# Kernel optimization log

Hardware: AMD Instinct MI355X
Metric: run time of the kernel (lower is better)

## Reference

```python
import jax, jax.numpy as jnp
import numpy as np

B, T, D_IN, EMB, H = 2, 2048, 1024, 1024, 16
HD = EMB // H  # head_dim = 64


def setup_inputs() -> dict:
    key = jax.random.key(0)
    ks = jax.random.split(key, 3)
    scale_qkv = 1.0 / np.sqrt(D_IN)
    scale_o = 1.0 / np.sqrt(EMB)
    return {
        "x": jax.random.normal(ks[0], (B, T, D_IN), dtype=jnp.float32),
        "W_qkv": jax.random.normal(ks[1], (D_IN, 3 * EMB), dtype=jnp.float32) * scale_qkv,
        "b_qkv": jnp.zeros((3 * EMB,), dtype=jnp.float32),
        "W_o": jax.random.normal(ks[2], (EMB, EMB), dtype=jnp.float32) * scale_o,
        "b_o": jnp.zeros((EMB,), dtype=jnp.float32),
    }


def reference(x, W_qkv, b_qkv, W_o, b_o):
    b, t, _ = x.shape
    qkv = x @ W_qkv + b_qkv                      # [B,T,3*EMB]
    # Match torch: reshape to (B,T,H,3*HD) -> permute -> chunk into q,k,v
    qkv = qkv.reshape(b, t, H, 3 * HD).transpose(0, 2, 1, 3)  # [B,H,T,3*HD]
    q, k, v = jnp.split(qkv, 3, axis=-1)         # each [B,H,T,HD]
    scale = 1.0 / jnp.sqrt(jnp.asarray(HD, dtype=q.dtype))
    scores = jnp.einsum("bhqd,bhkd->bhqk", q, k) * scale  # [B,H,T,T]
    attn = jax.nn.softmax(scores, axis=-1)
    values = jnp.einsum("bhqk,bhkd->bhqd", attn, v)       # [B,H,T,HD]
    values = values.transpose(0, 2, 1, 3).reshape(b, t, EMB)
    return values @ W_o + b_o
```

## Files before the change

### kernel.cpp

```cpp
#include <hip/hip_runtime.h>
#include <math.h>

typedef __bf16 bf16x8 __attribute__((ext_vector_type(8)));
typedef float f32x4 __attribute__((ext_vector_type(4)));
typedef short s16x4 __attribute__((ext_vector_type(4)));

#define GPTR(p) ((const __attribute__((address_space(1))) void*)(p))
#define LPTR(p) ((__attribute__((address_space(3))) void*)(p))

#define QSCALE 0.18033688011112042f

__device__ __forceinline__ unsigned short f2bf(float f) {
  unsigned int u = __float_as_uint(f);
  u += 0x7FFFu + ((u >> 16) & 1u);
  return (unsigned short)(u >> 16);
}

__device__ __forceinline__ unsigned int pack_bf2(float lo, float hi) {
  return __builtin_amdgcn_perm(__float_as_uint(hi) + 0x8000u,
                               __float_as_uint(lo) + 0x8000u, 0x07060302u);
}

__device__ __forceinline__ float fast_exp2(float x) {
#if __has_builtin(__builtin_amdgcn_exp2f)
  return __builtin_amdgcn_exp2f(x);
#else
  return exp2f(x);
#endif
}

__device__ __forceinline__ f32x4 zero4() {
  f32x4 z; z[0] = 0.f; z[1] = 0.f; z[2] = 0.f; z[3] = 0.f; return z;
}

__global__ void conv_x_bf16(const float* __restrict__ in, unsigned short* __restrict__ out) {
  int i = (blockIdx.x * 256 + threadIdx.x) * 4;
  float4 v = *(const float4*)(in + i);
  ushort4 o;
  o.x = f2bf(v.x); o.y = f2bf(v.y); o.z = f2bf(v.z); o.w = f2bf(v.w);
  *(ushort4*)(out + i) = o;
}

__global__ void transpose_conv(const float* __restrict__ in, unsigned short* __restrict__ out,
                               int K, int N) {
  __shared__ float tile[64][65];
  int k0 = blockIdx.y * 64, n0 = blockIdx.x * 64;
  int t = threadIdx.x;
#pragma unroll
  for (int p = 0; p < 16; ++p) {
    int l = p * 256 + t; int r = l >> 6, c = l & 63;
    tile[r][c] = in[(size_t)(k0 + r) * N + n0 + c];
  }
  __syncthreads();
#pragma unroll
  for (int p = 0; p < 16; ++p) {
    int l = p * 256 + t; int r = l >> 6, c = l & 63;
    out[(size_t)(n0 + r) * K + k0 + c] = f2bf(tile[c][r]);
  }
}

__global__ __launch_bounds__(256) void gemm_qkv(
    const unsigned short* __restrict__ A, const unsigned short* __restrict__ Bt,
    const float* __restrict__ bias,
    unsigned short* __restrict__ Qd, unsigned short* __restrict__ Kd,
    unsigned short* __restrict__ Vtd) {
  __shared__ unsigned short As[128 * 32];
  __shared__ unsigned short Bs[128 * 32];
  const int tid = threadIdx.x, wave = tid >> 6, lane = tid & 63;
  const int quad = lane >> 4, l16 = lane & 15;
  const int wm = (wave >> 1) * 64, wn = (wave & 1) * 64;
  const int m0 = blockIdx.y * 128, n0 = blockIdx.x * 128;
  f32x4 acc[4][4];
#pragma unroll
  for (int i = 0; i < 4; ++i)
#pragma unroll
    for (int j = 0; j < 4; ++j) acc[i][j] = zero4();

  const int c = wave * 64 + lane;
  const int rA = c >> 2, o16 = (c & 3) * 8;

  for (int k0 = 0; k0 < 1024; k0 += 32) {
    __syncthreads();
    __builtin_amdgcn_global_load_lds(GPTR(A + (size_t)(m0 + rA) * 1024 + k0 + o16),
                                     LPTR(As + wave * 512), 16, 0, 0);
    __builtin_amdgcn_global_load_lds(GPTR(A + (size_t)(m0 + 64 + rA) * 1024 + k0 + o16),
                                     LPTR(As + 2048 + wave * 512), 16, 0, 0);
    __builtin_amdgcn_global_load_lds(GPTR(Bt + (size_t)(n0 + rA) * 1024 + k0 + o16),
                                     LPTR(Bs + wave * 512), 16, 0, 0);
    __builtin_amdgcn_global_load_lds(GPTR(Bt + (size_t)(n0 + 64 + rA) * 1024 + k0 + o16),
                                     LPTR(Bs + 2048 + wave * 512), 16, 0, 0);
    __syncthreads();
    bf16x8 af[4], bfr[4];
#pragma unroll
    for (int mt = 0; mt < 4; ++mt)
      af[mt] = *(const bf16x8*)(As + (wm + mt * 16 + l16) * 32 + quad * 8);
#pragma unroll
    for (int nt = 0; nt < 4; ++nt)
      bfr[nt] = *(const bf16x8*)(Bs + (wn + nt * 16 + l16) * 32 + quad * 8);
#pragma unroll
    for (int mt = 0; mt < 4; ++mt)
#pragma unroll
      for (int nt = 0; nt < 4; ++nt)
        acc[mt][nt] = __builtin_amdgcn_mfma_f32_16x16x32_bf16(af[mt], bfr[nt], acc[mt][nt], 0, 0, 0);
  }

#pragma unroll
  for (int mt = 0; mt < 4; ++mt) {
#pragma unroll
    for (int nt = 0; nt < 4; ++nt) {
      int m = m0 + wm + mt * 16 + quad * 4;
      int n = n0 + wn + nt * 16 + l16;
      float bv = bias[n];
      int h = n / 192, rem = n - h * 192;
      int which = rem >> 6, d = rem & 63;
      int b = m >> 11, t0 = m & 2047;
      size_t head = (size_t)(b * 16 + h);
      f32x4 a = acc[mt][nt];
      if (which == 0) {
        size_t base = (head * 2048 + t0) * 64 + d;
#pragma unroll
        for (int i = 0; i < 4; ++i)
          Qd[base + (size_t)i * 64] = f2bf((a[i] + bv) * QSCALE);
      } else if (which == 1) {
        size_t base = head * 131072 + (size_t)(t0 >> 6) * 4096;
#pragma unroll
        for (int i = 0; i < 4; ++i) {
          int tt = t0 + i;
          Kd[base + (tt & 63) * 64 + (((d >> 3) ^ (tt & 7)) << 3) + (d & 7)] = f2bf(a[i] + bv);
        }
      } else {
        size_t base = head * 131072 + (size_t)(t0 >> 6) * 4096;
        ushort4 o;
        o.x = f2bf(a[0] + bv); o.y = f2bf(a[1] + bv);
        o.z = f2bf(a[2] + bv); o.w = f2bf(a[3] + bv);
        *(ushort4*)(Vtd + base + d * 64 + (((((t0 & 63) >> 3)) ^ (d & 7)) << 3) + (t0 & 7)) = o;
      }
    }
  }
}

__global__ __launch_bounds__(256) void flash_attn(
    const unsigned short* __restrict__ Qg,
    const unsigned short* __restrict__ Kg,
    const unsigned short* __restrict__ Vg,
    unsigned short* __restrict__ att) {
  __shared__ __align__(16) char smem[33792];
  unsigned short* Tb = (unsigned short*)smem;
  float* redO = (float*)smem;
  float* redL = (float*)(smem + 32768);
  const int tid = threadIdx.x, wave = tid >> 6, lane = tid & 63;
  const int quad = lane >> 4, l16 = lane & 15;
  const int h7 = l16 & 7;
  const int qhalf = wave >> 1, kh2 = wave & 1;
  const int bh = blockIdx.y;
  const int q0 = blockIdx.x * 128 + qhalf * 64;

  bf16x8 bq[4][2];
#pragma unroll
  for (int qg = 0; qg < 4; ++qg)
#pragma unroll
    for (int kh = 0; kh < 2; ++kh)
      bq[qg][kh] = *(const bf16x8*)(Qg + ((size_t)bh * 2048 + q0 + qg * 16 + l16) * 64 + kh * 32 + quad * 8);

  f32x4 o[4][4];
#pragma unroll
  for (int mt = 0; mt < 4; ++mt)
#pragma unroll
    for (int qg = 0; qg < 4; ++qg) o[mt][qg] = zero4();
  float lacc[4] = {0.f, 0.f, 0.f, 0.f};

  const unsigned short* Kt = Kg + (size_t)bh * 131072 + lane * 8;
  const unsigned short* Vt = Vg + (size_t)bh * 131072 + lane * 8;

  {
    unsigned short* Kb = Tb;
    __builtin_amdgcn_global_load_lds(GPTR(Kt + wave * 512),          LPTR(Kb + wave * 512), 16, 0, 0);
    __builtin_amdgcn_global_load_lds(GPTR(Kt + (4 + wave) * 512),    LPTR(Kb + (4 + wave) * 512), 16, 0, 0);
    __builtin_amdgcn_global_load_lds(GPTR(Vt + wave * 512),          LPTR(Kb + 4096 + wave * 512), 16, 0, 0);
    __builtin_amdgcn_global_load_lds(GPTR(Vt + (4 + wave) * 512),    LPTR(Kb + 4096 + (4 + wave) * 512), 16, 0, 0);
  }

  for (int tile = 0; tile < 32; ++tile) {
    __syncthreads();
    if (tile + 1 < 32) {
      unsigned short* Kb = Tb + ((tile + 1) & 1) * 8192;
      const unsigned short* Kg1 = Kt + (tile + 1) * 4096;
      const unsigned short* Vg1 = Vt + (tile + 1) * 4096;
      __builtin_amdgcn_global_load_lds(GPTR(Kg1 + wave * 512),       LPTR(Kb + wave * 512), 16, 0, 0);
      __builtin_amdgcn_global_load_lds(GPTR(Kg1 + (4 + wave) * 512), LPTR(Kb + (4 + wave) * 512), 16, 0, 0);
      __builtin_amdgcn_global_load_lds(GPTR(Vg1 + wave * 512),       LPTR(Kb + 4096 + wave * 512), 16, 0, 0);
      __builtin_amdgcn_global_load_lds(GPTR(Vg1 + (4 + wave) * 512), LPTR(Kb + 4096 + (4 + wave) * 512), 16, 0, 0);
    }
    const unsigned short* Ks = Tb + (tile & 1) * 8192;
    const unsigned short* Vs = Ks + 4096;

    f32x4 s[4][2];
#pragma unroll
    for (int qg = 0; qg < 4; ++qg)
#pragma unroll
      for (int kt = 0; kt < 2; ++kt) s[qg][kt] = zero4();
#pragma unroll
    for (int kt = 0; kt < 2; ++kt) {
      int krow = kh2 * 32 + kt * 16 + l16;
#pragma unroll
      for (int kh = 0; kh < 2; ++kh) {
        bf16x8 a = *(const bf16x8*)(Ks + krow * 64 + (((kh * 4 + quad) ^ h7) << 3));
#pragma unroll
        for (int qg = 0; qg < 4; ++qg)
          s[qg][kt] = __builtin_amdgcn_mfma_f32_16x16x32_bf16(a, bq[qg][kh], s[qg][kt], 0, 0, 0);
      }
    }

#pragma unroll
    for (int kt = 0; kt < 2; ++kt) {
      s16x4 pB[4];
#pragma unroll
      for (int qg = 0; qg < 4; ++qg) {
        float p0 = fast_exp2(s[qg][kt][0]);
        float p1 = fast_exp2(s[qg][kt][1]);
        float p2 = fast_exp2(s[qg][kt][2]);
        float p3 = fast_exp2(s[qg][kt][3]);
        lacc[qg] += (p0 + p1) + (p2 + p3);
        union { unsigned int u[2]; s16x4 v; } pk;
        pk.u[0] = pack_bf2(p0, p1);
        pk.u[1] = pack_bf2(p2, p3);
        pB[qg] = pk.v;
      }
      int cV = kh2 * 4 + kt * 2 + (quad >> 1);
#pragma unroll
      for (int mt = 0; mt < 4; ++mt) {
        s16x4 aV = *(const s16x4*)(Vs + (mt * 16 + l16) * 64 + ((cV ^ h7) << 3) + (quad & 1) * 4);
#pragma unroll
        for (int qg = 0; qg < 4; ++qg)
          o[mt][qg] = __builtin_amdgcn_mfma_f32_16x16x16bf16_1k(aV, pB[qg], o[mt][qg], 0, 0, 0);
      }
    }
  }

  float lfull[4];
#pragma unroll
  for (int qg = 0; qg < 4; ++qg) {
    float lw = lacc[qg];
    lw += __shfl_xor(lw, 16);
    lw += __shfl_xor(lw, 32);
    lfull[qg] = lw;
  }
  __syncthreads();
  if (kh2 == 1) {
    float* ob = redO + qhalf * 4096;
#pragma unroll
    for (int mt = 0; mt < 4; ++mt)
#pragma unroll
      for (int qg = 0; qg < 4; ++qg)
        *(f32x4*)(ob + ((qg * 4 + mt) * 4 + quad) * 64 + l16 * 4) = o[mt][qg];
    if (quad == 0) {
#pragma unroll
      for (int qg = 0; qg < 4; ++qg)
        redL[qhalf * 64 + qg * 16 + l16] = lfull[qg];
    }
  }
  __syncthreads();
  if (kh2 == 0) {
    int b = bh >> 4, h = bh & 15;
    float* ob = redO + qhalf * 4096;
#pragma unroll
    for (int qg = 0; qg < 4; ++qg) {
      float linv = 1.f / (lfull[qg] + redL[qhalf * 64 + qg * 16 + l16]);
      unsigned short* orow = att + ((size_t)b * 2048 + q0 + qg * 16 + l16) * 1024 + h * 64;
#pragma unroll
      for (int mt = 0; mt < 4; ++mt) {
        f32x4 part = *(const f32x4*)(ob + ((qg * 4 + mt) * 4 + quad) * 64 + l16 * 4);
        ushort4 ov;
        ov.x = f2bf((o[mt][qg][0] + part[0]) * linv);
        ov.y = f2bf((o[mt][qg][1] + part[1]) * linv);
        ov.z = f2bf((o[mt][qg][2] + part[2]) * linv);
        ov.w = f2bf((o[mt][qg][3] + part[3]) * linv);
        *(ushort4*)(orow + mt * 16 + quad * 4) = ov;
      }
    }
  }
}

__global__ __launch_bounds__(256) void gemm_out(
    const unsigned short* __restrict__ A, const unsigned short* __restrict__ Bt,
    const float* __restrict__ bias, float* __restrict__ out) {
  __shared__ unsigned short As[128 * 32];
  __shared__ unsigned short Bs[128 * 32];
  const int tid = threadIdx.x, wave = tid >> 6, lane = tid & 63;
  const int quad = lane >> 4, l16 = lane & 15;
  const int wm = (wave >> 1) * 64, wn = (wave & 1) * 64;
  const int m0 = blockIdx.y * 128, n0 = blockIdx.x * 128;
  f32x4 acc[4][4];
#pragma unroll
  for (int i = 0; i < 4; ++i)
#pragma unroll
    for (int j = 0; j < 4; ++j) acc[i][j] = zero4();

  const int c = wave * 64 + lane;
  const int rA = c >> 2, o16 = (c & 3) * 8;

  for (int k0 = 0; k0 < 1024; k0 += 32) {
    __syncthreads();
    __builtin_amdgcn_global_load_lds(GPTR(A + (size_t)(m0 + rA) * 1024 + k0 + o16),
                                     LPTR(As + wave * 512), 16, 0, 0);
    __builtin_amdgcn_global_load_lds(GPTR(A + (size_t)(m0 + 64 + rA) * 1024 + k0 + o16),
                                     LPTR(As + 2048 + wave * 512), 16, 0, 0);
    __builtin_amdgcn_global_load_lds(GPTR(Bt + (size_t)(n0 + rA) * 1024 + k0 + o16),
                                     LPTR(Bs + wave * 512), 16, 0, 0);
    __builtin_amdgcn_global_load_lds(GPTR(Bt + (size_t)(n0 + 64 + rA) * 1024 + k0 + o16),
                                     LPTR(Bs + 2048 + wave * 512), 16, 0, 0);
    __syncthreads();
    bf16x8 af[4], bfr[4];
#pragma unroll
    for (int mt = 0; mt < 4; ++mt)
      af[mt] = *(const bf16x8*)(As + (wm + mt * 16 + l16) * 32 + quad * 8);
#pragma unroll
    for (int nt = 0; nt < 4; ++nt)
      bfr[nt] = *(const bf16x8*)(Bs + (wn + nt * 16 + l16) * 32 + quad * 8);
#pragma unroll
    for (int mt = 0; mt < 4; ++mt)
#pragma unroll
      for (int nt = 0; nt < 4; ++nt)
        acc[mt][nt] = __builtin_amdgcn_mfma_f32_16x16x32_bf16(af[mt], bfr[nt], acc[mt][nt], 0, 0, 0);
  }

#pragma unroll
  for (int mt = 0; mt < 4; ++mt) {
#pragma unroll
    for (int nt = 0; nt < 4; ++nt) {
      int m = m0 + wm + mt * 16 + quad * 4;
      int n = n0 + wn + nt * 16 + l16;
      float bv = bias[n];
      float* orow = out + (size_t)m * 1024 + n;
      orow[0]        = acc[mt][nt][0] + bv;
      orow[1024]     = acc[mt][nt][1] + bv;
      orow[2 * 1024] = acc[mt][nt][2] + bv;
      orow[3 * 1024] = acc[mt][nt][3] + bv;
    }
  }
}

extern "C" void kernel_launch(void* const* d_in, const int* in_sizes, int n_in,
                              void* d_out, int out_size, void* d_ws, size_t ws_size,
                              hipStream_t stream) {
  const float* x    = (const float*)d_in[0];
  const float* Wqkv = (const float*)d_in[1];
  const float* bqkv = (const float*)d_in[2];
  const float* Wo   = (const float*)d_in[3];
  const float* bo   = (const float*)d_in[4];
  float* out = (float*)d_out;

  unsigned short* xb    = (unsigned short*)d_ws;
  unsigned short* wqkvt = xb    + (size_t)4096 * 1024;
  unsigned short* wot   = wqkvt + (size_t)3072 * 1024;
  unsigned short* Qd    = wot   + (size_t)1024 * 1024;
  unsigned short* Kd    = Qd    + (size_t)32 * 2048 * 64;
  unsigned short* Vtd   = Kd    + (size_t)32 * 2048 * 64;
  unsigned short* attb  = Vtd   + (size_t)32 * 2048 * 64;

  conv_x_bf16<<<4096, 256, 0, stream>>>(x, xb);
  transpose_conv<<<dim3(48, 16), 256, 0, stream>>>(Wqkv, wqkvt, 1024, 3072);
  transpose_conv<<<dim3(16, 16), 256, 0, stream>>>(Wo, wot, 1024, 1024);
  gemm_qkv<<<dim3(24, 32), 256, 0, stream>>>(xb, wqkvt, bqkv, Qd, Kd, Vtd);
  flash_attn<<<dim3(16, 32), 256, 0, stream>>>(Qd, Kd, Vtd, attb);
  gemm_out<<<dim3(8, 32), 256, 0, stream>>>(attb, wot, bo, out);
}
```

Measured before the change: 219.9 us.

## Split flash attention over key range with atomic fp32 partials and combine kernel

New measurement: 502.7 us. 2.29x slower.

```diff
diff --git a/kernel.cpp b/kernel.cpp
--- a/kernel.cpp
+++ b/kernel.cpp
@@ -139,11 +139,12 @@
   }
 }
 
-__global__ __launch_bounds__(256) void flash_attn(
+__global__ __launch_bounds__(256, 4) void flash_attn(
     const unsigned short* __restrict__ Qg,
     const unsigned short* __restrict__ Kg,
     const unsigned short* __restrict__ Vg,
-    unsigned short* __restrict__ att) {
+    float* __restrict__ pO,
+    float* __restrict__ pL) {
   __shared__ __align__(16) char smem[33792];
   unsigned short* Tb = (unsigned short*)smem;
   float* redO = (float*)smem;
@@ -154,6 +155,7 @@
   const int qhalf = wave >> 1, kh2 = wave & 1;
   const int bh = blockIdx.y;
   const int q0 = blockIdx.x * 128 + qhalf * 64;
+  const int tstart = blockIdx.z * 16, tend = tstart + 16;
 
   bf16x8 bq[4][2];
 #pragma unroll
@@ -173,16 +175,18 @@
   const unsigned short* Vt = Vg + (size_t)bh * 131072 + lane * 8;
 
   {
-    unsigned short* Kb = Tb;
-    __builtin_amdgcn_global_load_lds(GPTR(Kt + wave * 512),          LPTR(Kb + wave * 512), 16, 0, 0);
-    __builtin_amdgcn_global_load_lds(GPTR(Kt + (4 + wave) * 512),    LPTR(Kb + (4 + wave) * 512), 16, 0, 0);
-    __builtin_amdgcn_global_load_lds(GPTR(Vt + wave * 512),          LPTR(Kb + 4096 + wave * 512), 16, 0, 0);
-    __builtin_amdgcn_global_load_lds(GPTR(Vt + (4 + wave) * 512),    LPTR(Kb + 4096 + (4 + wave) * 512), 16, 0, 0);
-  }
-
-  for (int tile = 0; tile < 32; ++tile) {
-    __syncthreads();
-    if (tile + 1 < 32) {
+    unsigned short* Kb = Tb + (tstart & 1) * 8192;
+    const unsigned short* Kg0 = Kt + tstart * 4096;
+    const unsigned short* Vg0 = Vt + tstart * 4096;
+    __builtin_amdgcn_global_load_lds(GPTR(Kg0 + wave * 512),       LPTR(Kb + wave * 512), 16, 0, 0);
+    __builtin_amdgcn_global_load_lds(GPTR(Kg0 + (4 + wave) * 512), LPTR(Kb + (4 + wave) * 512), 16, 0, 0);
+    __builtin_amdgcn_global_load_lds(GPTR(Vg0 + wave * 512),       LPTR(Kb + 4096 + wave * 512), 16, 0, 0);
+    __builtin_amdgcn_global_load_lds(GPTR(Vg0 + (4 + wave) * 512), LPTR(Kb + 4096 + (4 + wave) * 512), 16, 0, 0);
+  }
+
+  for (int tile = tstart; tile < tend; ++tile) {
+    __syncthreads();
+    if (tile + 1 < tend) {
       unsigned short* Kb = Tb + ((tile + 1) & 1) * 8192;
       const unsigned short* Kg1 = Kt + (tile + 1) * 4096;
       const unsigned short* Vg1 = Vt + (tile + 1) * 4096;
@@ -261,24 +265,39 @@
   }
   __syncthreads();
   if (kh2 == 0) {
-    int b = bh >> 4, h = bh & 15;
     float* ob = redO + qhalf * 4096;
 #pragma unroll
     for (int qg = 0; qg < 4; ++qg) {
-      float linv = 1.f / (lfull[qg] + redL[qhalf * 64 + qg * 16 + l16]);
-      unsigned short* orow = att + ((size_t)b * 2048 + q0 + qg * 16 + l16) * 1024 + h * 64;
+      int q = q0 + qg * 16 + l16;
+      float lsum = lfull[qg] + redL[qhalf * 64 + qg * 16 + l16];
+      if (quad == 0) atomicAdd(pL + (size_t)bh * 2048 + q, lsum);
+      float* dst = pO + ((size_t)bh * 2048 + q) * 64;
 #pragma unroll
       for (int mt = 0; mt < 4; ++mt) {
         f32x4 part = *(const f32x4*)(ob + ((qg * 4 + mt) * 4 + quad) * 64 + l16 * 4);
-        ushort4 ov;
-        ov.x = f2bf((o[mt][qg][0] + part[0]) * linv);
-        ov.y = f2bf((o[mt][qg][1] + part[1]) * linv);
-        ov.z = f2bf((o[mt][qg][2] + part[2]) * linv);
-        ov.w = f2bf((o[mt][qg][3] + part[3]) * linv);
-        *(ushort4*)(orow + mt * 16 + quad * 4) = ov;
-      }
-    }
-  }
+        atomicAdd(dst + mt * 16 + quad * 4 + 0, o[mt][qg][0] + part[0]);
+        atomicAdd(dst + mt * 16 + quad * 4 + 1, o[mt][qg][1] + part[1]);
+        atomicAdd(dst + mt * 16 + quad * 4 + 2, o[mt][qg][2] + part[2]);
+        atomicAdd(dst + mt * 16 + quad * 4 + 3, o[mt][qg][3] + part[3]);
+      }
+    }
+  }
+}
+
+__global__ void attn_combine(const float* __restrict__ pO, const float* __restrict__ pL,
+                             unsigned short* __restrict__ att) {
+  size_t i = ((size_t)blockIdx.x * 256 + threadIdx.x);
+  size_t base = i * 4;
+  int d4 = (int)(base & 63);
+  size_t qq = base >> 6;
+  int bh = (int)(qq >> 11), q = (int)(qq & 2047);
+  float linv = 1.f / pL[qq];
+  float4 v = *(const float4*)(pO + base);
+  int b = bh >> 4, h = bh & 15;
+  ushort4 ov;
+  ov.x = f2bf(v.x * linv); ov.y = f2bf(v.y * linv);
+  ov.z = f2bf(v.z * linv); ov.w = f2bf(v.w * linv);
+  *(ushort4*)(att + ((size_t)b * 2048 + q) * 1024 + h * 64 + d4) = ov;
 }
 
 __global__ __launch_bounds__(256) void gemm_out(
@@ -351,17 +370,22 @@
   float* out = (float*)d_out;
 
   unsigned short* xb    = (unsigned short*)d_ws;
-  unsigned short* wqkvt = xb    + (size_t)4096 * 1024;
-  unsigned short* wot   = wqkvt + (size_t)3072 * 1024;
-  unsigned short* Qd    = wot   + (size_t)1024 * 1024;
-  unsigned short* Kd    = Qd    + (size_t)32 * 2048 * 64;
-  unsigned short* Vtd   = Kd    + (size_t)32 * 2048 * 64;
-  unsigned short* attb  = Vtd   + (size_t)32 * 2048 * 64;
+  unsigned short* wqkvt = xb + (size_t)4096 * 1024;
+  float*          pO    = (float*)d_ws;
+  unsigned short* Qd    = (unsigned short*)((char*)d_ws + (size_t)16 * 1024 * 1024);
+  unsigned short* Kd    = Qd   + (size_t)32 * 2048 * 64;
+  unsigned short* Vtd   = Kd   + (size_t)32 * 2048 * 64;
+  unsigned short* attb  = Vtd  + (size_t)32 * 2048 * 64;
+  unsigned short* wot   = attb + (size_t)4096 * 1024;
+  float*          pL    = (float*)(wot + (size_t)1024 * 1024);
 
   conv_x_bf16<<<4096, 256, 0, stream>>>(x, xb);
   transpose_conv<<<dim3(48, 16), 256, 0, stream>>>(Wqkv, wqkvt, 1024, 3072);
   transpose_conv<<<dim3(16, 16), 256, 0, stream>>>(Wo, wot, 1024, 1024);
   gemm_qkv<<<dim3(24, 32), 256, 0, stream>>>(xb, wqkvt, bqkv, Qd, Kd, Vtd);
-  flash_attn<<<dim3(16, 32), 256, 0, stream>>>(Qd, Kd, Vtd, attb);
+  hipMemsetAsync(pO, 0, (size_t)32 * 2048 * 64 * 4, stream);
+  hipMemsetAsync(pL, 0, (size_t)32 * 2048 * 4, stream);
+  flash_attn<<<dim3(16, 32, 2), 256, 0, stream>>>(Qd, Kd, Vtd, pO, pL);
+  attn_combine<<<4096, 256, 0, stream>>>(pO, pL, attb);
   gemm_out<<<dim3(8, 32), 256, 0, stream>>>(attb, wot, bo, out);
 }
```
